# Optimization experiments

Hardware: AMD Instinct MI355X
Metric: run time of the kernel (lower is better)

## Reference

```python
import jax, jax.numpy as jnp
import numpy as np

N_HEAD, D_MODEL, D_K, D_V, D_O = 16, 1024, 64, 64, 1024
B, S = 4, 2048


def setup_inputs() -> dict:
    key = jax.random.key(0)
    ks = jax.random.split(key, 11)
    s = 0.02
    return {
        "q": jax.random.normal(ks[0], (B, S, D_MODEL), jnp.float32),
        "k": jax.random.normal(ks[1], (B, S, D_MODEL), jnp.float32),
        "v": jax.random.normal(ks[2], (B, S, D_MODEL), jnp.float32),
        "Wq": jax.random.normal(ks[3], (D_MODEL, N_HEAD * D_K), jnp.float32) * s,
        "bq": jnp.zeros((N_HEAD * D_K,), jnp.float32),
        "Wk": jax.random.normal(ks[4], (D_MODEL, N_HEAD * D_K), jnp.float32) * s,
        "bk": jnp.zeros((N_HEAD * D_K,), jnp.float32),
        "Wv": jax.random.normal(ks[5], (D_MODEL, N_HEAD * D_V), jnp.float32) * s,
        "bv": jnp.zeros((N_HEAD * D_V,), jnp.float32),
        "Wo": jax.random.normal(ks[6], (N_HEAD * D_V, D_O), jnp.float32) * s,
        "bo": jnp.zeros((D_O,), jnp.float32),
    }


def reference(q, k, v, Wq, bq, Wk, bk, Wv, bv, Wo, bo):
    b, n_q, _ = q.shape
    # QKV projections -> [b, s, h, d]
    qh = (q @ Wq + bq).reshape(b, -1, N_HEAD, D_K)
    kh = (k @ Wk + bk).reshape(b, -1, N_HEAD, D_K)
    vh = (v @ Wv + bv).reshape(b, -1, N_HEAD, D_V)
    scale = jnp.asarray(np.power(D_K, 0.5), qh.dtype)
    # scores [b, h, n_q, n_k]
    scores = jnp.einsum("bqhd,bkhd->bhqk", qh, kh) / scale
    attn = jax.nn.softmax(scores, axis=-1)
    out = jnp.einsum("bhqk,bkhd->bqhd", attn, vh).reshape(b, n_q, N_HEAD * D_V)
    return out @ Wo + bo
```

## Files before the change

### kernel.cpp

```cpp
#include <hip/hip_runtime.h>
#include <hip/hip_bf16.h>


typedef __attribute__((ext_vector_type(8))) short bf16x8;
typedef __attribute__((ext_vector_type(4))) float f32x4;
typedef __attribute__((ext_vector_type(4))) unsigned short u16x4;

#define QSCALE 0.1803368801111244f

__device__ __forceinline__ unsigned short f2bf(float x) {
  unsigned u = __builtin_bit_cast(unsigned, x);
  u += 0x7fffu + ((u >> 16) & 1u);
  return (unsigned short)(u >> 16);
}

__device__ __forceinline__ short f2bf_s(float x) {
  __hip_bfloat16 h = __float2bfloat16(x);
  return __builtin_bit_cast(short, h);
}

__device__ __forceinline__ float fexp2(float x) {
#if __has_builtin(__builtin_amdgcn_exp2f)
  return __builtin_amdgcn_exp2f(x);
#else
  return exp2f(x);
#endif
}

__device__ __forceinline__ void gload16(const void* g, void* l) {
  __builtin_amdgcn_global_load_lds(
      (const __attribute__((address_space(1))) unsigned int*)g,
      (__attribute__((address_space(3))) unsigned int*)l, 16, 0, 0);
}

__global__ void wtrans4(const float* __restrict__ W0, const float* __restrict__ W1,
                        const float* __restrict__ W2, const float* __restrict__ W3,
                        unsigned short* __restrict__ WT) {
  __shared__ float t[32][33];
  int x = threadIdx.x, y = threadIdx.y;
  int k0 = blockIdx.x * 32, n0 = blockIdx.y * 32;
  int z = blockIdx.z;
  const float* W = z == 0 ? W0 : z == 1 ? W1 : z == 2 ? W2 : W3;
  float scale = z == 0 ? QSCALE : 1.0f;
  unsigned short* dst = WT + (size_t)z * (1024 * 1024);
#pragma unroll
  for (int i = 0; i < 4; i++)
    t[y + i * 8][x] = W[(k0 + y + i * 8) * 1024 + n0 + x];
  __syncthreads();
#pragma unroll
  for (int i = 0; i < 4; i++)
    dst[(n0 + y + i * 8) * 1024 + k0 + x] = f2bf(t[x][y + i * 8] * scale);
}

template <bool AF32, int MODE>
__global__ __launch_bounds__(256, 2) void gemm128(
    const void* __restrict__ Ap, const unsigned short* __restrict__ BT,
    const float* __restrict__ bias, float bscale, void* __restrict__ Cp) {
  __shared__ __align__(16) char As[8192];
  __shared__ __align__(16) char Bs[8192];
  const int K = 1024;
  int tid = threadIdx.x;
  int lane = tid & 63;
  int w = tid >> 6;
  int wr = w >> 1, wc = w & 1;
  int bid = blockIdx.x;
  int sid = (bid & 7) * 64 + (bid >> 3);
  int m0 = (sid >> 3) * 128, n0 = (sid & 7) * 128;

  int p0 = w * 2048 + lane * 16;
  int p1 = p0 + 1024;
  int row0 = p0 >> 6, col0 = (p0 & 63) ^ (((p0 >> 7) & 3) << 4);
  int row1 = p1 >> 6, col1 = (p1 & 63) ^ (((p1 >> 7) & 3) << 4);
  const char* srcB0 = (const char*)BT + (size_t)(n0 + row0) * 2048 + col0;
  const char* srcB1 = (const char*)BT + (size_t)(n0 + row1) * 2048 + col1;
  const char* srcA0 = (const char*)Ap + (size_t)(m0 + row0) * 2048 + col0;
  const char* srcA1 = (const char*)Ap + (size_t)(m0 + row1) * 2048 + col1;

  int r = tid >> 1;
  int kb = (tid & 1) << 4;
  int wbyte = r * 64 + (kb << 1);
  int amask = ((r >> 1) & 3) << 4;

  f32x4 acc[4][4];
#pragma unroll
  for (int i = 0; i < 4; i++)
#pragma unroll
    for (int j = 0; j < 4; j++) acc[i][j] = (f32x4){0.f, 0.f, 0.f, 0.f};

  const float* Af = (const float*)Ap;
  f32x4 afr[4];
  if (AF32) {
    const f32x4* p = (const f32x4*)(Af + (size_t)(m0 + r) * K + kb);
#pragma unroll
    for (int i = 0; i < 4; i++) afr[i] = p[i];
  }

  int cc = lane & 15, g = lane >> 4;

  for (int k0 = 0; k0 < K; k0 += 32) {
    __syncthreads();
    if (AF32) {
      bf16x8 s0, s1;
#pragma unroll
      for (int i = 0; i < 8; i++) {
        s0[i] = (short)f2bf(afr[i >> 2][i & 3]);
        s1[i] = (short)f2bf(afr[2 + (i >> 2)][i & 3]);
      }
      *(bf16x8*)(As + (wbyte ^ amask)) = s0;
      *(bf16x8*)(As + ((wbyte + 16) ^ amask)) = s1;
    } else {
      gload16(srcA0 + k0 * 2, As + w * 2048);
      gload16(srcA1 + k0 * 2, As + w * 2048 + 1024);
    }
    gload16(srcB0 + k0 * 2, Bs + w * 2048);
    gload16(srcB1 + k0 * 2, Bs + w * 2048 + 1024);
    __syncthreads();
    if (AF32 && k0 + 32 < K) {
      const f32x4* p = (const f32x4*)(Af + (size_t)(m0 + r) * K + k0 + 32 + kb);
#pragma unroll
      for (int i = 0; i < 4; i++) afr[i] = p[i];
    }
    bf16x8 a[4], b[4];
#pragma unroll
    for (int mi = 0; mi < 4; mi++) {
      int row = wr * 64 + mi * 16 + cc;
      int x = row * 64 + g * 16;
      a[mi] = *(const bf16x8*)(As + (x ^ (((row >> 1) & 3) << 4)));
    }
#pragma unroll
    for (int ni = 0; ni < 4; ni++) {
      int row = wc * 64 + ni * 16 + cc;
      int x = row * 64 + g * 16;
      b[ni] = *(const bf16x8*)(Bs + (x ^ (((row >> 1) & 3) << 4)));
    }
#pragma unroll
    for (int mi = 0; mi < 4; mi++)
#pragma unroll
      for (int ni = 0; ni < 4; ni++)
        acc[mi][ni] =
            __builtin_amdgcn_mfma_f32_16x16x32_bf16(a[mi], b[ni], acc[mi][ni], 0, 0, 0);
  }

#pragma unroll
  for (int ni = 0; ni < 4; ni++) {
    int n = n0 + wc * 64 + ni * 16 + cc;
    float bv = bias[n] * bscale;
#pragma unroll
    for (int mi = 0; mi < 4; mi++) {
      int mbase = m0 + wr * 64 + mi * 16 + g * 4;
      if (MODE == 2) {
        u16x4 pk;
#pragma unroll
        for (int j = 0; j < 4; j++) pk[j] = f2bf(acc[mi][ni][j] + bv);
        int bb = mbase >> 11, s = mbase & 2047;
        int sp = (s & ~31) | ((((s & 15) >> 2) << 3) + (((s >> 4) & 1) << 2));
        int hh = n >> 6, d = n & 63;
        *(u16x4*)&((unsigned short*)Cp)[(((size_t)(bb * 16 + hh) * 64 + d) << 11) + sp] = pk;
      } else {
#pragma unroll
        for (int j = 0; j < 4; j++) {
          float val = acc[mi][ni][j] + bv;
          int m = mbase + j;
          if (MODE == 0) {
            int bb = m >> 11, s = m & 2047;
            int hh = n >> 6, d = n & 63;
            ((unsigned short*)Cp)[(((bb * 16 + hh) * 2048 + s) << 6) + d] = f2bf(val);
          } else {
            ((float*)Cp)[(size_t)m * 1024 + n] = val;
          }
        }
      }
    }
  }
}

__global__ __launch_bounds__(256, 4) void attn64(
    const unsigned short* __restrict__ Qh, const unsigned short* __restrict__ Kh,
    const unsigned short* __restrict__ Vt, unsigned short* __restrict__ O) {
  __shared__ __align__(16) char Ks[2][8192];
  __shared__ __align__(16) char Vs[2][8192];
  int tid = threadIdx.x, lane = tid & 63, w = tid >> 6;
  int bid = blockIdx.x;
  int sid = (bid & 7) * 128 + (bid >> 3);
  int bh = sid >> 4, qb = sid & 15;
  int b = bh >> 4, h = bh & 15;
  const unsigned short* Q  = Qh + (size_t)bh * (2048 * 64);
  const unsigned short* Kb = Kh + (size_t)bh * (2048 * 64);
  const unsigned short* Vb = Vt + (size_t)bh * (64 * 2048);
  int q0 = qb * 128 + w * 32;
  int cc = lane & 15, g = lane >> 4, g4 = g << 2;

  bf16x8 vones;
#pragma unroll
  for (int i = 0; i < 8; i++) vones[i] = (short)0x3F80;

  bf16x8 aq0[2], aq1[2];
#pragma unroll
  for (int g2 = 0; g2 < 2; g2++) {
    aq0[g2] = *(const bf16x8*)(Q + (size_t)(q0 + cc) * 64 + g2 * 32 + g * 8);
    aq1[g2] = *(const bf16x8*)(Q + (size_t)(q0 + 16 + cc) * 64 + g2 * 32 + g * 8);
  }

  f32x4 oacc0[4], oacc1[4];
#pragma unroll
  for (int df = 0; df < 4; df++) {
    oacc0[df] = (f32x4){0.f, 0.f, 0.f, 0.f};
    oacc1[df] = (f32x4){0.f, 0.f, 0.f, 0.f};
  }
  f32x4 lacc0 = (f32x4){0.f, 0.f, 0.f, 0.f};
  f32x4 lacc1 = (f32x4){0.f, 0.f, 0.f, 0.f};

  int kr = tid >> 2, kq = tid & 3;
  int kswz = (kr & 7) << 4;
  int kbyte = kr * 128 + kq * 32;

  bf16x8 kv[2], vv[2];
  {
    const bf16x8* pK = (const bf16x8*)(Kb + (size_t)kr * 64 + kq * 16);
    const bf16x8* pV = (const bf16x8*)(Vb + (size_t)kr * 2048 + kq * 16);
    kv[0] = pK[0]; kv[1] = pK[1];
    vv[0] = pV[0]; vv[1] = pV[1];
  }
#pragma unroll
  for (int i = 0; i < 2; i++) {
    *(bf16x8*)(Ks[0] + ((kbyte + i * 16) ^ kswz)) = kv[i];
    *(bf16x8*)(Vs[0] + ((kbyte + i * 16) ^ kswz)) = vv[i];
  }
  int cur = 0;

  for (int kt = 0; kt < 2048; kt += 64) {
    __syncthreads();
    if (kt + 64 < 2048) {
      const bf16x8* pK = (const bf16x8*)(Kb + (size_t)(kt + 64 + kr) * 64 + kq * 16);
      const bf16x8* pV = (const bf16x8*)(Vb + (size_t)kr * 2048 + kt + 64 + kq * 16);
      kv[0] = pK[0]; kv[1] = pK[1];
      vv[0] = pV[0]; vv[1] = pV[1];
    }
    const char* Kc = Ks[cur];
    const char* Vc = Vs[cur];

    f32x4 sc0[4], sc1[4];
#pragma unroll
    for (int nf = 0; nf < 4; nf++) {
      sc0[nf] = (f32x4){0.f, 0.f, 0.f, 0.f};
      sc1[nf] = (f32x4){0.f, 0.f, 0.f, 0.f};
    }
    __builtin_amdgcn_s_setprio(1);
#pragma unroll
    for (int nf = 0; nf < 4; nf++) {
#pragma unroll
      for (int g2 = 0; g2 < 2; g2++) {
        int rk = nf * 16 + cc;
        int byte = (rk * 128 + g2 * 64 + g * 16) ^ ((rk & 7) << 4);
        bf16x8 bk = *(const bf16x8*)(Kc + byte);
        sc0[nf] = __builtin_amdgcn_mfma_f32_16x16x32_bf16(bk, aq0[g2], sc0[nf], 0, 0, 0);
        sc1[nf] = __builtin_amdgcn_mfma_f32_16x16x32_bf16(bk, aq1[g2], sc1[nf], 0, 0, 0);
      }
    }
    __builtin_amdgcn_s_setprio(0);

#pragma unroll
    for (int nf = 0; nf < 4; nf++)
#pragma unroll
      for (int t = 0; t < 4; t++) {
        sc0[nf][t] = fexp2(sc0[nf][t]);
        sc1[nf][t] = fexp2(sc1[nf][t]);
      }

    bf16x8 pa0[2], pa1[2];
#pragma unroll
    for (int kk = 0; kk < 2; kk++) {
#pragma unroll
      for (int i = 0; i < 4; i++) {
        pa0[kk][i]     = f2bf_s(sc0[2 * kk][i]);
        pa0[kk][4 + i] = f2bf_s(sc0[2 * kk + 1][i]);
        pa1[kk][i]     = f2bf_s(sc1[2 * kk][i]);
        pa1[kk][4 + i] = f2bf_s(sc1[2 * kk + 1][i]);
      }
    }
    __builtin_amdgcn_s_setprio(1);
#pragma unroll
    for (int df = 0; df < 4; df++) {
#pragma unroll
      for (int kk = 0; kk < 2; kk++) {
        int rv = df * 16 + cc;
        int byte = (rv * 128 + kk * 64 + g * 16) ^ ((rv & 7) << 4);
        bf16x8 bv = *(const bf16x8*)(Vc + byte);
        oacc0[df] = __builtin_amdgcn_mfma_f32_16x16x32_bf16(pa0[kk], bv, oacc0[df], 0, 0, 0);
        oacc1[df] = __builtin_amdgcn_mfma_f32_16x16x32_bf16(pa1[kk], bv, oacc1[df], 0, 0, 0);
      }
    }
#pragma unroll
    for (int kk = 0; kk < 2; kk++) {
      lacc0 = __builtin_amdgcn_mfma_f32_16x16x32_bf16(pa0[kk], vones, lacc0, 0, 0, 0);
      lacc1 = __builtin_amdgcn_mfma_f32_16x16x32_bf16(pa1[kk], vones, lacc1, 0, 0, 0);
    }
    __builtin_amdgcn_s_setprio(0);

    if (kt + 64 < 2048) {
      char* Kn = Ks[cur ^ 1];
      char* Vn = Vs[cur ^ 1];
#pragma unroll
      for (int i = 0; i < 2; i++) {
        *(bf16x8*)(Kn + ((kbyte + i * 16) ^ kswz)) = kv[i];
        *(bf16x8*)(Vn + ((kbyte + i * 16) ^ kswz)) = vv[i];
      }
    }
    cur ^= 1;
  }

#pragma unroll
  for (int t = 0; t < 4; t++) {
    float inv0 = 1.0f / lacc0[t];
    float inv1 = 1.0f / lacc1[t];
    int srow = q0 + g4 + t;
#pragma unroll
    for (int df = 0; df < 4; df++) {
      int d = df * 16 + cc;
      O[((size_t)b * 2048 + srow) * 1024 + h * 64 + d]      = f2bf(oacc0[df][t] * inv0);
      O[((size_t)b * 2048 + srow + 16) * 1024 + h * 64 + d] = f2bf(oacc1[df][t] * inv1);
    }
  }
}

extern "C" void kernel_launch(void* const* d_in, const int* in_sizes, int n_in,
                              void* d_out, int out_size, void* d_ws, size_t ws_size,
                              hipStream_t stream) {
  const float* q  = (const float*)d_in[0];
  const float* k  = (const float*)d_in[1];
  const float* v  = (const float*)d_in[2];
  const float* Wq = (const float*)d_in[3];
  const float* bq = (const float*)d_in[4];
  const float* Wk = (const float*)d_in[5];
  const float* bk = (const float*)d_in[6];
  const float* Wv = (const float*)d_in[7];
  const float* bv = (const float*)d_in[8];
  const float* Wo = (const float*)d_in[9];
  const float* bo = (const float*)d_in[10];

  char* ws = (char*)d_ws;
  const size_t MB = 1024 * 1024;
  unsigned short* WqT = (unsigned short*)(ws + 0 * MB);
  unsigned short* WkT = (unsigned short*)(ws + 2 * MB);
  unsigned short* WvT = (unsigned short*)(ws + 4 * MB);
  unsigned short* WoT = (unsigned short*)(ws + 6 * MB);
  unsigned short* qh  = (unsigned short*)(ws + 8 * MB);
  unsigned short* kh  = (unsigned short*)(ws + 24 * MB);
  unsigned short* vt  = (unsigned short*)(ws + 40 * MB);
  unsigned short* ao  = (unsigned short*)(ws + 56 * MB);

  wtrans4<<<dim3(32, 32, 4), dim3(32, 8), 0, stream>>>(Wq, Wk, Wv, Wo, WqT);

  gemm128<true, 0><<<512, 256, 0, stream>>>(q, WqT, bq, QSCALE, qh);
  gemm128<true, 0><<<512, 256, 0, stream>>>(k, WkT, bk, 1.0f, kh);
  gemm128<true, 2><<<512, 256, 0, stream>>>(v, WvT, bv, 1.0f, vt);

  attn64<<<1024, 256, 0, stream>>>(qh, kh, vt, ao);

  gemm128<false, 1><<<512, 256, 0, stream>>>(ao, WoT, bo, 1.0f, d_out);
}
```

Baseline: 224.9 us.

## Double K-tile to 64 and prefetch GEMM operands through registers

The projection GEMM moves from direct global-to-LDS loads with a 32-wide K step to register-staged prefetch of both A and B with a 64-wide K step. The next tile's global loads are issued before the barrier so they overlap the MFMA work, and each barrier pair now covers twice as many MFMAs. The LDS swizzle is changed to match the 128-byte rows. In exchange, LDS per block doubles to 32KB and register pressure rises (8 f32x4 plus 8 bf16x8 prefetch registers), which may reduce occupancy under launch_bounds(256,2).

```diff
diff --git a/kernel.cpp b/kernel.cpp
--- a/kernel.cpp
+++ b/kernel.cpp
@@ -25,12 +25,6 @@
 #else
   return exp2f(x);
 #endif
-}
-
-__device__ __forceinline__ void gload16(const void* g, void* l) {
-  __builtin_amdgcn_global_load_lds(
-      (const __attribute__((address_space(1))) unsigned int*)g,
-      (__attribute__((address_space(3))) unsigned int*)l, 16, 0, 0);
 }
 
 __global__ void wtrans4(const float* __restrict__ W0, const float* __restrict__ W1,
@@ -56,8 +50,8 @@
 __global__ __launch_bounds__(256, 2) void gemm128(
     const void* __restrict__ Ap, const unsigned short* __restrict__ BT,
     const float* __restrict__ bias, float bscale, void* __restrict__ Cp) {
-  __shared__ __align__(16) char As[8192];
-  __shared__ __align__(16) char Bs[8192];
+  __shared__ __align__(16) char As[16384];
+  __shared__ __align__(16) char Bs[16384];
   const int K = 1024;
   int tid = threadIdx.x;
   int lane = tid & 63;
@@ -66,20 +60,10 @@
   int bid = blockIdx.x;
   int sid = (bid & 7) * 64 + (bid >> 3);
   int m0 = (sid >> 3) * 128, n0 = (sid & 7) * 128;
-
-  int p0 = w * 2048 + lane * 16;
-  int p1 = p0 + 1024;
-  int row0 = p0 >> 6, col0 = (p0 & 63) ^ (((p0 >> 7) & 3) << 4);
-  int row1 = p1 >> 6, col1 = (p1 & 63) ^ (((p1 >> 7) & 3) << 4);
-  const char* srcB0 = (const char*)BT + (size_t)(n0 + row0) * 2048 + col0;
-  const char* srcB1 = (const char*)BT + (size_t)(n0 + row1) * 2048 + col1;
-  const char* srcA0 = (const char*)Ap + (size_t)(m0 + row0) * 2048 + col0;
-  const char* srcA1 = (const char*)Ap + (size_t)(m0 + row1) * 2048 + col1;
-
   int r = tid >> 1;
-  int kb = (tid & 1) << 4;
-  int wbyte = r * 64 + (kb << 1);
-  int amask = ((r >> 1) & 3) << 4;
+  int kb = (tid & 1) << 5;
+  int wbyte = r * 128 + ((tid & 1) << 6);
+  int swz = (r & 7) << 4;
 
   f32x4 acc[4][4];
 #pragma unroll
@@ -88,57 +72,87 @@
     for (int j = 0; j < 4; j++) acc[i][j] = (f32x4){0.f, 0.f, 0.f, 0.f};
 
   const float* Af = (const float*)Ap;
-  f32x4 afr[4];
+  const unsigned short* Ab = (const unsigned short*)Ap;
+
+  f32x4 afr[8];
+  bf16x8 afb[4];
+  bf16x8 bfr[4];
+
   if (AF32) {
     const f32x4* p = (const f32x4*)(Af + (size_t)(m0 + r) * K + kb);
 #pragma unroll
-    for (int i = 0; i < 4; i++) afr[i] = p[i];
+    for (int i = 0; i < 8; i++) afr[i] = p[i];
+  } else {
+    const bf16x8* p = (const bf16x8*)(Ab + (size_t)(m0 + r) * K + kb);
+#pragma unroll
+    for (int i = 0; i < 4; i++) afb[i] = p[i];
+  }
+  {
+    const bf16x8* p = (const bf16x8*)(BT + (size_t)(n0 + r) * K + kb);
+#pragma unroll
+    for (int i = 0; i < 4; i++) bfr[i] = p[i];
   }
 
   int cc = lane & 15, g = lane >> 4;
 
-  for (int k0 = 0; k0 < K; k0 += 32) {
+  for (int k0 = 0; k0 < K; k0 += 64) {
     __syncthreads();
     if (AF32) {
-      bf16x8 s0, s1;
-#pragma unroll
-      for (int i = 0; i < 8; i++) {
-        s0[i] = (short)f2bf(afr[i >> 2][i & 3]);
-        s1[i] = (short)f2bf(afr[2 + (i >> 2)][i & 3]);
-      }
-      *(bf16x8*)(As + (wbyte ^ amask)) = s0;
-      *(bf16x8*)(As + ((wbyte + 16) ^ amask)) = s1;
+#pragma unroll
+      for (int c = 0; c < 4; c++) {
+        bf16x8 s;
+#pragma unroll
+        for (int i = 0; i < 4; i++) {
+          s[i] = (short)f2bf(afr[2 * c][i]);
+          s[4 + i] = (short)f2bf(afr[2 * c + 1][i]);
+        }
+        *(bf16x8*)(As + ((wbyte + c * 16) ^ swz)) = s;
+      }
     } else {
-      gload16(srcA0 + k0 * 2, As + w * 2048);
-      gload16(srcA1 + k0 * 2, As + w * 2048 + 1024);
-    }
-    gload16(srcB0 + k0 * 2, Bs + w * 2048);
-    gload16(srcB1 + k0 * 2, Bs + w * 2048 + 1024);
+#pragma unroll
+      for (int c = 0; c < 4; c++)
+        *(bf16x8*)(As + ((wbyte + c * 16) ^ swz)) = afb[c];
+    }
+#pragma unroll
+    for (int c = 0; c < 4; c++)
+      *(bf16x8*)(Bs + ((wbyte + c * 16) ^ swz)) = bfr[c];
+    if (k0 + 64 < K) {
+      if (AF32) {
+        const f32x4* p = (const f32x4*)(Af + (size_t)(m0 + r) * K + k0 + 64 + kb);
+#pragma unroll
+        for (int i = 0; i < 8; i++) afr[i] = p[i];
+      } else {
+        const bf16x8* p = (const bf16x8*)(Ab + (size_t)(m0 + r) * K + k0 + 64 + kb);
+#pragma unroll
+        for (int i = 0; i < 4; i++) afb[i] = p[i];
+      }
+      const bf16x8* p = (const bf16x8*)(BT + (size_t)(n0 + r) * K + k0 + 64 + kb);
+#pragma unroll
+      for (int i = 0; i < 4; i++) bfr[i] = p[i];
+    }
     __syncthreads();
-    if (AF32 && k0 + 32 < K) {
-      const f32x4* p = (const f32x4*)(Af + (size_t)(m0 + r) * K + k0 + 32 + kb);
-#pragma unroll
-      for (int i = 0; i < 4; i++) afr[i] = p[i];
-    }
-    bf16x8 a[4], b[4];
-#pragma unroll
-    for (int mi = 0; mi < 4; mi++) {
-      int row = wr * 64 + mi * 16 + cc;
-      int x = row * 64 + g * 16;
-      a[mi] = *(const bf16x8*)(As + (x ^ (((row >> 1) & 3) << 4)));
-    }
-#pragma unroll
-    for (int ni = 0; ni < 4; ni++) {
-      int row = wc * 64 + ni * 16 + cc;
-      int x = row * 64 + g * 16;
-      b[ni] = *(const bf16x8*)(Bs + (x ^ (((row >> 1) & 3) << 4)));
-    }
-#pragma unroll
-    for (int mi = 0; mi < 4; mi++)
-#pragma unroll
-      for (int ni = 0; ni < 4; ni++)
-        acc[mi][ni] =
-            __builtin_amdgcn_mfma_f32_16x16x32_bf16(a[mi], b[ni], acc[mi][ni], 0, 0, 0);
+#pragma unroll
+    for (int kk = 0; kk < 2; kk++) {
+      bf16x8 a[4], b[4];
+#pragma unroll
+      for (int mi = 0; mi < 4; mi++) {
+        int row = wr * 64 + mi * 16 + cc;
+        int x = row * 128 + kk * 64 + g * 16;
+        a[mi] = *(const bf16x8*)(As + (x ^ ((row & 7) << 4)));
+      }
+#pragma unroll
+      for (int ni = 0; ni < 4; ni++) {
+        int row = wc * 64 + ni * 16 + cc;
+        int x = row * 128 + kk * 64 + g * 16;
+        b[ni] = *(const bf16x8*)(Bs + (x ^ ((row & 7) << 4)));
+      }
+#pragma unroll
+      for (int mi = 0; mi < 4; mi++)
+#pragma unroll
+        for (int ni = 0; ni < 4; ni++)
+          acc[mi][ni] =
+              __builtin_amdgcn_mfma_f32_16x16x32_bf16(a[mi], b[ni], acc[mi][ni], 0, 0, 0);
+    }
   }
 
 #pragma unroll
```

New measurement: 240.3 us. +6.8%, slower.

## Stage GEMM operand tiles through registers with prefetch instead of direct-to-LDS loads

Applied to the files above, without the earlier changes.

The GEMM kernel stops using global_load_lds for the bf16 A and B tiles. It now loads each thread's next K-slice into registers, writes the current slice to LDS with ordinary stores, and issues the prefetch for the following iteration before the barrier, so global latency can overlap the MFMA work. The LDS XOR swizzle changes from a 2-row-period pattern to one keyed on row&7, applied the same way on write and read. This costs extra VGPRs and explicit LDS store instructions in exchange for software prefetch, and it may hurt occupancy under the 256x2 launch bounds.

```diff
diff --git a/kernel.cpp b/kernel.cpp
--- a/kernel.cpp
+++ b/kernel.cpp
@@ -25,12 +25,6 @@
 #else
   return exp2f(x);
 #endif
-}
-
-__device__ __forceinline__ void gload16(const void* g, void* l) {
-  __builtin_amdgcn_global_load_lds(
-      (const __attribute__((address_space(1))) unsigned int*)g,
-      (__attribute__((address_space(3))) unsigned int*)l, 16, 0, 0);
 }
 
 __global__ void wtrans4(const float* __restrict__ W0, const float* __restrict__ W1,
@@ -66,20 +60,8 @@
   int bid = blockIdx.x;
   int sid = (bid & 7) * 64 + (bid >> 3);
   int m0 = (sid >> 3) * 128, n0 = (sid & 7) * 128;
-
-  int p0 = w * 2048 + lane * 16;
-  int p1 = p0 + 1024;
-  int row0 = p0 >> 6, col0 = (p0 & 63) ^ (((p0 >> 7) & 3) << 4);
-  int row1 = p1 >> 6, col1 = (p1 & 63) ^ (((p1 >> 7) & 3) << 4);
-  const char* srcB0 = (const char*)BT + (size_t)(n0 + row0) * 2048 + col0;
-  const char* srcB1 = (const char*)BT + (size_t)(n0 + row1) * 2048 + col1;
-  const char* srcA0 = (const char*)Ap + (size_t)(m0 + row0) * 2048 + col0;
-  const char* srcA1 = (const char*)Ap + (size_t)(m0 + row1) * 2048 + col1;
-
   int r = tid >> 1;
   int kb = (tid & 1) << 4;
-  int wbyte = r * 64 + (kb << 1);
-  int amask = ((r >> 1) & 3) << 4;
 
   f32x4 acc[4][4];
 #pragma unroll
@@ -88,13 +70,27 @@
     for (int j = 0; j < 4; j++) acc[i][j] = (f32x4){0.f, 0.f, 0.f, 0.f};
 
   const float* Af = (const float*)Ap;
+  const unsigned short* Ab = (const unsigned short*)Ap;
+
   f32x4 afr[4];
+  bf16x8 afb[2];
+  bf16x8 bfr[2];
+
   if (AF32) {
     const f32x4* p = (const f32x4*)(Af + (size_t)(m0 + r) * K + kb);
 #pragma unroll
     for (int i = 0; i < 4; i++) afr[i] = p[i];
-  }
-
+  } else {
+    const bf16x8* p = (const bf16x8*)(Ab + (size_t)(m0 + r) * K + kb);
+    afb[0] = p[0]; afb[1] = p[1];
+  }
+  {
+    const bf16x8* p = (const bf16x8*)(BT + (size_t)(n0 + r) * K + kb);
+    bfr[0] = p[0]; bfr[1] = p[1];
+  }
+
+  int swz = (r & 7) << 4;
+  int wbyte = r * 64 + kb * 2;
   int cc = lane & 15, g = lane >> 4;
 
   for (int k0 = 0; k0 < K; k0 += 32) {
@@ -106,32 +102,39 @@
         s0[i] = (short)f2bf(afr[i >> 2][i & 3]);
         s1[i] = (short)f2bf(afr[2 + (i >> 2)][i & 3]);
       }
-      *(bf16x8*)(As + (wbyte ^ amask)) = s0;
-      *(bf16x8*)(As + ((wbyte + 16) ^ amask)) = s1;
+      *(bf16x8*)(As + (wbyte ^ swz)) = s0;
+      *(bf16x8*)(As + ((wbyte + 16) ^ swz)) = s1;
     } else {
-      gload16(srcA0 + k0 * 2, As + w * 2048);
-      gload16(srcA1 + k0 * 2, As + w * 2048 + 1024);
-    }
-    gload16(srcB0 + k0 * 2, Bs + w * 2048);
-    gload16(srcB1 + k0 * 2, Bs + w * 2048 + 1024);
+      *(bf16x8*)(As + (wbyte ^ swz)) = afb[0];
+      *(bf16x8*)(As + ((wbyte + 16) ^ swz)) = afb[1];
+    }
+    *(bf16x8*)(Bs + (wbyte ^ swz)) = bfr[0];
+    *(bf16x8*)(Bs + ((wbyte + 16) ^ swz)) = bfr[1];
+    if (k0 + 32 < K) {
+      if (AF32) {
+        const f32x4* p = (const f32x4*)(Af + (size_t)(m0 + r) * K + k0 + 32 + kb);
+#pragma unroll
+        for (int i = 0; i < 4; i++) afr[i] = p[i];
+      } else {
+        const bf16x8* p = (const bf16x8*)(Ab + (size_t)(m0 + r) * K + k0 + 32 + kb);
+        afb[0] = p[0]; afb[1] = p[1];
+      }
+      const bf16x8* p = (const bf16x8*)(BT + (size_t)(n0 + r) * K + k0 + 32 + kb);
+      bfr[0] = p[0]; bfr[1] = p[1];
+    }
     __syncthreads();
-    if (AF32 && k0 + 32 < K) {
-      const f32x4* p = (const f32x4*)(Af + (size_t)(m0 + r) * K + k0 + 32 + kb);
-#pragma unroll
-      for (int i = 0; i < 4; i++) afr[i] = p[i];
-    }
     bf16x8 a[4], b[4];
 #pragma unroll
     for (int mi = 0; mi < 4; mi++) {
       int row = wr * 64 + mi * 16 + cc;
-      int x = row * 64 + g * 16;
-      a[mi] = *(const bf16x8*)(As + (x ^ (((row >> 1) & 3) << 4)));
+      int byte = (row * 64 + g * 16) ^ ((row & 7) << 4);
+      a[mi] = *(const bf16x8*)(As + byte);
     }
 #pragma unroll
     for (int ni = 0; ni < 4; ni++) {
       int row = wc * 64 + ni * 16 + cc;
-      int x = row * 64 + g * 16;
-      b[ni] = *(const bf16x8*)(Bs + (x ^ (((row >> 1) & 3) << 4)));
+      int byte = (row * 64 + g * 16) ^ ((row & 7) << 4);
+      b[ni] = *(const bf16x8*)(Bs + byte);
     }
 #pragma unroll
     for (int mi = 0; mi < 4; mi++)
```

Measured after the change: 205.9 us. 8.5% less time.
